# Kernel optimization log

Hardware: AMD Instinct MI355X
Metric: run time of the kernel (lower is better)

Reference implementation:

```python
import jax, jax.numpy as jnp
import numpy as np

BATCH, SEQ, EMBED = 4, 4096, 512
NUM_HEADS = 8
D_K = EMBED // NUM_HEADS  # = n_wires of the quantum layer


def setup_inputs() -> dict:
    key = jax.random.key(0)
    k1, k2, k3, k4 = jax.random.split(key, 4)
    x = jax.random.normal(k1, (BATCH, SEQ, EMBED), dtype=jnp.float32)
    theta = jax.random.normal(k2, (D_K,), dtype=jnp.float32)          # trainable RX angles (shared across heads)
    W_out = jax.random.normal(k3, (EMBED, EMBED), dtype=jnp.float32) * (1.0 / np.sqrt(EMBED))
    b_out = jax.random.normal(k4, (EMBED,), dtype=jnp.float32) * 0.01
    return {"x": x, "theta": theta, "W_out": W_out, "b_out": b_out}


def reference(x, theta, W_out, b_out):
    b, s, e = x.shape
    d_k = theta.shape[0]
    h = e // d_k
    # Quantum stage: per wire, RX(x_i) then RX(theta_i) on |0>, measure PauliZ.
    # RX gates on the same wire compose, and <Z| RX(phi)|0> state> = cos(phi),
    # so the whole per-head circuit is elementwise cos(x + theta).
    xh = x.reshape(b, s, h, d_k)                 # split heads
    q_concat = jnp.cos(xh + theta).reshape(b, s, e)
    # q = k = v = out_proj(q_concat)  (same Linear applied three times)
    q = q_concat @ W_out.T + b_out               # [b, s, e]
    scale = 1.0 / jnp.sqrt(jnp.asarray(d_k, dtype=q.dtype))
    scores = jax.nn.softmax(jnp.einsum('bie,bje->bij', q, q) * scale, axis=-1)  # [b, s, s]
    out = jnp.einsum('bij,bje->bie', scores, q)  # dropout = identity (inference)
    return out
```

## Files before the change

kernel.cpp:

```cpp
#include <hip/hip_runtime.h>

typedef __bf16 bf16_t;
typedef bf16_t bf16x8 __attribute__((ext_vector_type(8)));
typedef bf16_t bf16x4 __attribute__((ext_vector_type(4)));
typedef float f32x4 __attribute__((ext_vector_type(4)));

#define BATCH 4
#define SEQ 4096
#define EMBED 512
#define MTOT (BATCH * SEQ)
#define NSPLIT 2
#define KT (SEQ / NSPLIT)
#define BC 32
#define FITERS (KT / BC)

__device__ float  Lacc_g[MTOT];
__device__ bf16_t Wbf_g[EMBED * EMBED];

__device__ __forceinline__ void async_copy16(const bf16_t* g, bf16_t* l) {
    __builtin_amdgcn_global_load_lds(
        (const __attribute__((address_space(1))) unsigned int*)g,
        (__attribute__((address_space(3))) unsigned int*)l, 16, 0, 0);
}

__global__ __launch_bounds__(256) void cvt_w_kernel(const float* __restrict__ W) {
    const int i = (blockIdx.x * 256 + threadIdx.x) * 4;
    float4 v = *(const float4*)&W[i];
    bf16x4 o;
    o[0] = (bf16_t)v.x; o[1] = (bf16_t)v.y; o[2] = (bf16_t)v.z; o[3] = (bf16_t)v.w;
    *(bf16x4*)&Wbf_g[i] = o;
    if (blockIdx.x < 16)
        ((float4*)Lacc_g)[blockIdx.x * 256 + threadIdx.x] = make_float4(0.f, 0.f, 0.f, 0.f);
}

__global__ __launch_bounds__(256) void cvt_a_kernel(
    const float* __restrict__ x, const float* __restrict__ theta,
    bf16_t* __restrict__ abuf)
{
    const int i = (blockIdx.x * 256 + threadIdx.x) * 8;
    float4 a = *(const float4*)&x[i];
    float4 b = *(const float4*)&x[i + 4];
    const int e0 = i & 63;
    bf16x8 o;
    o[0] = (bf16_t)__cosf(a.x + theta[e0 + 0]);
    o[1] = (bf16_t)__cosf(a.y + theta[e0 + 1]);
    o[2] = (bf16_t)__cosf(a.z + theta[e0 + 2]);
    o[3] = (bf16_t)__cosf(a.w + theta[e0 + 3]);
    o[4] = (bf16_t)__cosf(b.x + theta[e0 + 4]);
    o[5] = (bf16_t)__cosf(b.y + theta[e0 + 5]);
    o[6] = (bf16_t)__cosf(b.z + theta[e0 + 6]);
    o[7] = (bf16_t)__cosf(b.w + theta[e0 + 7]);
    *(bf16x8*)&abuf[i] = o;
}

__global__ __launch_bounds__(256, 2) void gemm_q_kernel(
    const bf16_t* __restrict__ abuf, const float* __restrict__ bias,
    bf16_t* __restrict__ kperm, bf16_t* __restrict__ qt)
{
    __shared__ alignas(16) bf16_t As[128 * 64];
    __shared__ alignas(16) bf16_t Bs[128 * 64];

    const int t    = threadIdx.x;
    const int lane = t & 63;
    const int wave = t >> 6;
    const int l15  = lane & 15;
    const int quad = lane >> 4;
    const int m0   = (blockIdx.x >> 2) * 128;
    const int n0   = (blockIdx.x & 3) * 128;
    const int wm   = wave >> 1;
    const int wn   = wave & 1;

    const int drow = lane >> 3;
    const int dseg = lane & 7;
    const int sseg = dseg ^ drow;

    f32x4 acc[4][4];
#pragma unroll
    for (int mt = 0; mt < 4; ++mt)
#pragma unroll
        for (int nt = 0; nt < 4; ++nt) acc[mt][nt] = (f32x4){0.f, 0.f, 0.f, 0.f};

    for (int kk = 0; kk < 8; ++kk) {
        const int k0 = kk * 64;
        __syncthreads();
#pragma unroll
        for (int j = 0; j < 4; ++j) {
            const int c   = wave * 4 + j;
            const int row = c * 8 + drow;
            async_copy16(&abuf[(size_t)(m0 + row) * 512 + k0 + sseg * 8], &As[c * 512]);
            async_copy16(&Wbf_g[(size_t)(n0 + row) * 512 + k0 + sseg * 8], &Bs[c * 512]);
        }
        __syncthreads();
#pragma unroll
        for (int kh = 0; kh < 2; ++kh) {
            bf16x8 af[4], bfr[4];
#pragma unroll
            for (int i = 0; i < 4; ++i) {
                const int rA = wm * 64 + i * 16 + l15;
                const int rB = wn * 64 + i * 16 + l15;
                const int sg = kh * 4 + quad;
                af[i]  = *(const bf16x8*)&As[rA * 64 + (sg ^ (rA & 7)) * 8];
                bfr[i] = *(const bf16x8*)&Bs[rB * 64 + (sg ^ (rB & 7)) * 8];
            }
#pragma unroll
            for (int mt = 0; mt < 4; ++mt)
#pragma unroll
                for (int nt = 0; nt < 4; ++nt)
                    acc[mt][nt] = __builtin_amdgcn_mfma_f32_16x16x32_bf16(af[mt], bfr[nt], acc[mt][nt], 0, 0, 0);
        }
    }

#pragma unroll
    for (int nt = 0; nt < 4; ++nt) {
        const int col = n0 + wn * 64 + nt * 16 + l15;
        const float bv = bias[col];
        const int kf = col >> 5;
        const int qk = (col >> 3) & 3;
        const int jj = col & 7;
#pragma unroll
        for (int mt = 0; mt < 4; ++mt) {
            const int row0 = m0 + wm * 64 + mt * 16 + quad * 4;
            const int b    = row0 >> 12;
            const int i0   = row0 & 4095;
            const int tile = i0 >> 5;
            const size_t kb = (size_t)b * (SEQ * EMBED) + (size_t)tile * 16384
                            + (size_t)(((i0 >> 4) & 1) * 16 + kf) * 512 + qk * 128
                            + (i0 & 15) * 8 + jj;
            bf16x4 pack;
#pragma unroll
            for (int r = 0; r < 4; ++r) {
                bf16_t qv = (bf16_t)(acc[mt][nt][r] + bv);
                kperm[kb + r * 8] = qv;
                pack[r] = qv;
            }
            *(bf16x4*)&qt[((size_t)(b * 512 + col) << 12) + i0] = pack;
        }
    }
}

__global__ __launch_bounds__(256, 2) void flash_kernel(
    const bf16_t* __restrict__ kp, const bf16_t* __restrict__ qt,
    float* __restrict__ out)
{
    __shared__ alignas(16) bf16_t Ks[2][32 * 512];
    __shared__ alignas(16) bf16_t Ps[2][4 * 512];

    const int t    = threadIdx.x;
    const int lane = t & 63;
    const int wave = t >> 6;
    const int l15  = lane & 15;
    const int quad = lane >> 4;

    const int L      = blockIdx.x;
    const int g      = L & 7;
    const int qtile  = L >> 3;
    const int batch  = g >> 1;
    const int ksplit = g & 1;

    const int q0     = qtile * 64;
    const int kbase  = ksplit * KT;
    const int ktile0 = kbase >> 5;
    const bf16_t* kpb = kp + (size_t)batch * SEQ * EMBED;
    const bf16_t* qtb = qt + (size_t)batch * EMBED * SEQ;

#pragma unroll
    for (int cc = 0; cc < 8; ++cc) {
        const int f = cc * 4 + wave;
        async_copy16(&kpb[(size_t)ktile0 * 16384 + f * 512 + lane * 8],
                     &Ks[0][f * 512]);
    }

    bf16x8 bQ[16];
    {
        const size_t qb = (size_t)(qtile * 2 + (wave >> 1)) * 16384
                        + (size_t)(wave & 1) * 16 * 512;
#pragma unroll
        for (int kf = 0; kf < 16; ++kf)
            bQ[kf] = *(const bf16x8*)&kpb[qb + kf * 512 + quad * 128 + l15 * 8];
    }

    f32x4 O[4][8];
#pragma unroll
    for (int m = 0; m < 4; ++m)
#pragma unroll
        for (int n = 0; n < 8; ++n) O[m][n] = (f32x4){0.f, 0.f, 0.f, 0.f};
    float lpart = 0.f;

    for (int it = 0; it < FITERS; ++it) {
        const int cbuf = it & 1;
        const int pbuf = cbuf ^ 1;
        __syncthreads();
        if (it + 1 < FITERS) {
#pragma unroll
            for (int cc = 0; cc < 8; ++cc) {
                const int f = cc * 4 + wave;
                async_copy16(&kpb[(size_t)(ktile0 + it + 1) * 16384 + f * 512 + lane * 8],
                             &Ks[pbuf][f * 512]);
            }
        }
        bf16x8 bv[8];
        if (it) {
            const int kv = kbase + (it - 1) * BC;
#pragma unroll
            for (int n = 0; n < 8; ++n)
                bv[n] = *(const bf16x8*)&qtb[(size_t)(wave * 128 + n * 16 + l15) * 4096
                                             + kv + quad * 8];
        }
        f32x4 s[2];
#pragma unroll
        for (int kt = 0; kt < 2; ++kt) {
            f32x4 a = (f32x4){0.f, 0.f, 0.f, 0.f};
#pragma unroll
            for (int kf = 0; kf < 16; ++kf) {
                bf16x8 ak = *(const bf16x8*)&Ks[cbuf][(kt * 16 + kf) * 512 + lane * 8];
                a = __builtin_amdgcn_mfma_f32_16x16x32_bf16(ak, bQ[kf], a, 0, 0, 0);
            }
            s[kt] = a;
        }
#pragma unroll
        for (int kt = 0; kt < 2; ++kt) {
            bf16x4 pk;
#pragma unroll
            for (int r = 0; r < 4; ++r) {
                bf16_t pb = (bf16_t)__expf(s[kt][r] * 0.125f);
                lpart += (float)pb;
                pk[r] = pb;
            }
            *(bf16x4*)&Ps[cbuf][wave * 512 + (kt * 2 + (quad >> 1)) * 128
                                + l15 * 8 + (quad & 1) * 4] = pk;
        }
        if (it) {
            bf16x8 pa[4];
#pragma unroll
            for (int mt = 0; mt < 4; ++mt)
                pa[mt] = *(const bf16x8*)&Ps[pbuf][mt * 512 + lane * 8];
#pragma unroll
            for (int n = 0; n < 8; ++n)
#pragma unroll
                for (int mt = 0; mt < 4; ++mt)
                    O[mt][n] = __builtin_amdgcn_mfma_f32_16x16x32_bf16(pa[mt], bv[n], O[mt][n], 0, 0, 0);
        }
    }
    __syncthreads();
    {
        const int pbuf = (FITERS - 1) & 1;
        const int kv = kbase + (FITERS - 1) * BC;
        bf16x8 bv[8];
#pragma unroll
        for (int n = 0; n < 8; ++n)
            bv[n] = *(const bf16x8*)&qtb[(size_t)(wave * 128 + n * 16 + l15) * 4096
                                         + kv + quad * 8];
        bf16x8 pa[4];
#pragma unroll
        for (int mt = 0; mt < 4; ++mt)
            pa[mt] = *(const bf16x8*)&Ps[pbuf][mt * 512 + lane * 8];
#pragma unroll
        for (int n = 0; n < 8; ++n)
#pragma unroll
            for (int mt = 0; mt < 4; ++mt)
                O[mt][n] = __builtin_amdgcn_mfma_f32_16x16x32_bf16(pa[mt], bv[n], O[mt][n], 0, 0, 0);
    }

    {
        float ls = lpart;
        ls += __shfl_xor(ls, 16);
        ls += __shfl_xor(ls, 32);
        if (quad == 0)
            atomicAdd(&Lacc_g[batch * SEQ + q0 + wave * 16 + l15], ls);
    }
#pragma unroll
    for (int mt = 0; mt < 4; ++mt)
#pragma unroll
        for (int r = 0; r < 4; ++r) {
            const size_t row = (size_t)batch * SEQ + q0 + mt * 16 + quad * 4 + r;
#pragma unroll
            for (int n = 0; n < 8; ++n)
                atomicAdd(&out[row * 512 + wave * 128 + n * 16 + l15], O[mt][n][r]);
        }
}

__global__ __launch_bounds__(256) void norm_kernel(float* __restrict__ out)
{
    const int idx = blockIdx.x * 256 + threadIdx.x;
    float4 v = ((float4*)out)[idx];
    const float inv = 1.0f / Lacc_g[idx >> 7];
    v.x *= inv; v.y *= inv; v.z *= inv; v.w *= inv;
    ((float4*)out)[idx] = v;
}

extern "C" void kernel_launch(void* const* d_in, const int* in_sizes, int n_in,
                              void* d_out, int out_size, void* d_ws, size_t ws_size,
                              hipStream_t stream) {
    const float* x     = (const float*)d_in[0];
    const float* theta = (const float*)d_in[1];
    const float* W     = (const float*)d_in[2];
    const float* bias  = (const float*)d_in[3];
    float* out    = (float*)d_out;
    bf16_t* kperm = (bf16_t*)d_ws;
    bf16_t* qt    = kperm + (size_t)MTOT * EMBED;
    bf16_t* abuf  = qt + (size_t)MTOT * EMBED;

    hipMemsetAsync(out, 0, (size_t)MTOT * EMBED * sizeof(float), stream);

    cvt_w_kernel<<<dim3(EMBED * EMBED / 4 / 256), dim3(256), 0, stream>>>(W);

    cvt_a_kernel<<<dim3(MTOT * EMBED / 8 / 256), dim3(256), 0, stream>>>(x, theta, abuf);

    gemm_q_kernel<<<dim3((MTOT / 128) * 4), dim3(256), 0, stream>>>(abuf, bias, kperm, qt);

    flash_kernel<<<dim3(64 * BATCH * NSPLIT), dim3(256), 0, stream>>>(kperm, qt, out);

    norm_kernel<<<dim3(MTOT * EMBED / 4 / 256), dim3(256), 0, stream>>>(out);
}
```

Baseline: 378.7 us.

## Stage GEMM epilogue through LDS for coalesced stores; reorder loads and raise MFMA priority

The projection GEMM epilogue now writes results into a padded LDS buffer and then stores both the permuted K layout and the transposed Q layout with 16-byte coalesced writes. Previously it did scattered 2-byte stores. In the flash kernel, the V-fragment global loads are issued before the async K-tile copies, and the PV MFMA block is wrapped in s_setprio to favour matrix issue. The added LDS (about 34KB) may reduce occupancy of the GEMM kernel, and extra barriers are added to the epilogue.

```diff
diff --git a/kernel.cpp b/kernel.cpp
--- a/kernel.cpp
+++ b/kernel.cpp
@@ -59,6 +59,7 @@
 {
     __shared__ alignas(16) bf16_t As[128 * 64];
     __shared__ alignas(16) bf16_t Bs[128 * 64];
+    __shared__ alignas(16) bf16_t Es[128 * 136];
 
     const int t    = threadIdx.x;
     const int lane = t & 63;
@@ -110,30 +111,65 @@
         }
     }
 
+    const int b     = m0 >> 12;
+    const int mloc  = m0 & 4095;
+
 #pragma unroll
     for (int nt = 0; nt < 4; ++nt) {
-        const int col = n0 + wn * 64 + nt * 16 + l15;
-        const float bv = bias[col];
-        const int kf = col >> 5;
-        const int qk = (col >> 3) & 3;
-        const int jj = col & 7;
+        const int colL = wn * 64 + nt * 16 + l15;
+        const float bv = bias[n0 + colL];
+        const int kfL = colL >> 5;
+        const int inc = ((colL >> 3) & 3) * 128 + (colL & 7);
 #pragma unroll
         for (int mt = 0; mt < 4; ++mt) {
-            const int row0 = m0 + wm * 64 + mt * 16 + quad * 4;
-            const int b    = row0 >> 12;
-            const int i0   = row0 & 4095;
-            const int tile = i0 >> 5;
-            const size_t kb = (size_t)b * (SEQ * EMBED) + (size_t)tile * 16384
-                            + (size_t)(((i0 >> 4) & 1) * 16 + kf) * 512 + qk * 128
-                            + (i0 & 15) * 8 + jj;
-            bf16x4 pack;
-#pragma unroll
-            for (int r = 0; r < 4; ++r) {
-                bf16_t qv = (bf16_t)(acc[mt][nt][r] + bv);
-                kperm[kb + r * 8] = qv;
-                pack[r] = qv;
-            }
-            *(bf16x4*)&qt[((size_t)(b * 512 + col) << 12) + i0] = pack;
+            const int rowL0 = wm * 64 + mt * 16 + quad * 4;
+            const int c     = (rowL0 >> 5) * 8 + ((rowL0 >> 4) & 1) * 4 + kfL;
+            const int base  = c * 512 + inc + (rowL0 & 15) * 8;
+#pragma unroll
+            for (int r = 0; r < 4; ++r)
+                Es[base + r * 8] = (bf16_t)(acc[mt][nt][r] + bv);
+        }
+    }
+    __syncthreads();
+    {
+        const int tileB = mloc >> 5;
+        const int kfB   = n0 >> 5;
+#pragma unroll
+        for (int p = 0; p < 8; ++p) {
+            const int flat = p * 256 + t;
+            const int c2   = flat >> 6;
+            const int off  = (flat & 63) * 8;
+            const int tile = c2 >> 3;
+            const int mh   = (c2 >> 2) & 1;
+            const int kfL2 = c2 & 3;
+            const size_t dst = (size_t)b * (SEQ * EMBED)
+                             + (size_t)(tileB + tile) * 16384
+                             + (size_t)(mh * 16 + kfB + kfL2) * 512 + off;
+            *(bf16x8*)&kperm[dst] = *(const bf16x8*)&Es[c2 * 512 + off];
+        }
+    }
+    __syncthreads();
+#pragma unroll
+    for (int nt = 0; nt < 4; ++nt) {
+        const int colL = wn * 64 + nt * 16 + l15;
+        const float bv = bias[n0 + colL];
+#pragma unroll
+        for (int mt = 0; mt < 4; ++mt) {
+            const int rowL0 = wm * 64 + mt * 16 + quad * 4;
+#pragma unroll
+            for (int r = 0; r < 4; ++r)
+                Es[colL * 136 + rowL0 + r] = (bf16_t)(acc[mt][nt][r] + bv);
+        }
+    }
+    __syncthreads();
+    {
+#pragma unroll
+        for (int p = 0; p < 8; ++p) {
+            const int flat = p * 256 + t;
+            const int col  = flat >> 4;
+            const int sub  = flat & 15;
+            *(bf16x8*)&qt[((size_t)(b * 512 + n0 + col) << 12) + mloc + sub * 8]
+                = *(const bf16x8*)&Es[col * 136 + sub * 8];
         }
     }
 }
@@ -190,6 +226,14 @@
         const int cbuf = it & 1;
         const int pbuf = cbuf ^ 1;
         __syncthreads();
+        bf16x8 bv[8];
+        if (it) {
+            const int kv = kbase + (it - 1) * BC;
+#pragma unroll
+            for (int n = 0; n < 8; ++n)
+                bv[n] = *(const bf16x8*)&qtb[(size_t)(wave * 128 + n * 16 + l15) * 4096
+                                             + kv + quad * 8];
+        }
         if (it + 1 < FITERS) {
 #pragma unroll
             for (int cc = 0; cc < 8; ++cc) {
@@ -197,14 +241,6 @@
                 async_copy16(&kpb[(size_t)(ktile0 + it + 1) * 16384 + f * 512 + lane * 8],
                              &Ks[pbuf][f * 512]);
             }
-        }
-        bf16x8 bv[8];
-        if (it) {
-            const int kv = kbase + (it - 1) * BC;
-#pragma unroll
-            for (int n = 0; n < 8; ++n)
-                bv[n] = *(const bf16x8*)&qtb[(size_t)(wave * 128 + n * 16 + l15) * 4096
-                                             + kv + quad * 8];
         }
         f32x4 s[2];
 #pragma unroll
@@ -234,11 +270,13 @@
 #pragma unroll
             for (int mt = 0; mt < 4; ++mt)
                 pa[mt] = *(const bf16x8*)&Ps[pbuf][mt * 512 + lane * 8];
+            __builtin_amdgcn_s_setprio(1);
 #pragma unroll
             for (int n = 0; n < 8; ++n)
 #pragma unroll
                 for (int mt = 0; mt < 4; ++mt)
                     O[mt][n] = __builtin_amdgcn_mfma_f32_16x16x32_bf16(pa[mt], bv[n], O[mt][n], 0, 0, 0);
+            __builtin_amdgcn_s_setprio(0);
         }
     }
     __syncthreads();
@@ -254,11 +292,13 @@
 #pragma unroll
         for (int mt = 0; mt < 4; ++mt)
             pa[mt] = *(const bf16x8*)&Ps[pbuf][mt * 512 + lane * 8];
+        __builtin_amdgcn_s_setprio(1);
 #pragma unroll
         for (int n = 0; n < 8; ++n)
 #pragma unroll
             for (int mt = 0; mt < 4; ++mt)
                 O[mt][n] = __builtin_amdgcn_mfma_f32_16x16x32_bf16(pa[mt], bv[n], O[mt][n], 0, 0, 0);
+        __builtin_amdgcn_s_setprio(0);
     }
 
     {
```

After: 366.1 us. 1.03x faster.
